# Optimization experiments

Hardware: AMD Instinct MI355X
Metric: run time of the kernel (lower is better)

Reference implementation:

```python
import math
import jax, jax.numpy as jnp
import numpy as np

HOP = 256
N_FFT = 1024
SR = 24000
B = 8
T = 1200          # feature frames
L = T * HOP       # 307200 audio samples
K_REV = 8192
BINS = N_FFT // 2 + 1


def setup_inputs() -> dict:
    key = jax.random.key(0)
    k1, k2, k3, k4, k5 = jax.random.split(key, 5)
    # realistic voiced f0 in [50, 400] Hz (forward gates on f0 > 20 Hz)
    f0 = 50.0 + 350.0 * jax.random.uniform(k1, (B, T), dtype=jnp.float32)
    env_per = jax.random.uniform(k2, (B, BINS, T), dtype=jnp.float32)
    env_noi = 0.1 * jax.random.uniform(k3, (B, BINS, T), dtype=jnp.float32)
    rev = 0.01 * jax.random.normal(k4, (B, K_REV), dtype=jnp.float32)
    # stands in for torch.rand_like(imp) inside forward (uniform [0,1))
    noi = jax.random.uniform(k5, (B, L), dtype=jnp.float32)
    # periodic Hann window, as torch.hann_window(n_fft)
    window = (0.5 - 0.5 * jnp.cos(2.0 * jnp.pi * jnp.arange(N_FFT) / N_FFT)).astype(jnp.float32)
    return {"f0": f0, "env_per": env_per, "env_noi": env_noi, "rev": rev, "noi": noi, "window": window}


def _interp_linear(x, scale):
    # torch F.interpolate(mode='linear', align_corners=False)
    Lx = x.shape[-1]
    out_len = Lx * scale
    src = (jnp.arange(out_len, dtype=jnp.float32) + 0.5) / scale - 0.5
    src = jnp.clip(src, 0.0, Lx - 1)
    i0 = jnp.floor(src).astype(jnp.int32)
    i1 = jnp.minimum(i0 + 1, Lx - 1)
    w = src - i0.astype(jnp.float32)
    return x[:, i0] * (1.0 - w) + x[:, i1] * w


def _stft(x, window):
    # torch.stft(center=True, pad_mode='reflect', return_complex=True)
    pad = N_FFT // 2
    xp = jnp.pad(x, ((0, 0), (pad, pad)), mode='reflect')
    n_frames = 1 + (xp.shape[-1] - N_FFT) // HOP
    idx = jnp.arange(n_frames)[:, None] * HOP + jnp.arange(N_FFT)[None, :]
    frames = xp[:, idx] * window                      # [B, F, N_FFT]
    return jnp.fft.rfft(frames, axis=-1).transpose(0, 2, 1)  # [B, BINS, F]


def _istft(spec, window):
    # torch.istft(center=True): windowed overlap-add with window-square normalization
    frames = jnp.fft.irfft(spec.transpose(0, 2, 1), n=N_FFT, axis=-1) * window  # [B, F, N_FFT]
    Bc, Fr, _ = frames.shape
    out_len = N_FFT + HOP * (Fr - 1)
    idx = (jnp.arange(Fr)[:, None] * HOP + jnp.arange(N_FFT)[None, :]).reshape(-1)
    out = jnp.zeros((Bc, out_len), frames.dtype).at[:, idx].add(frames.reshape(Bc, -1))
    wsq = jnp.zeros((out_len,), frames.dtype).at[idx].add(jnp.tile(window ** 2, Fr))
    out = out / jnp.where(wsq > 1e-11, wsq, 1.0)
    pad = N_FFT // 2
    return out[:, pad:out_len - pad]


def _min_phase(amp, eps=1e-5):
    # homomorphic minimum-phase reconstruction from real amplitude envelope
    # amp: [B, BINS, F]  ->  complex spectrum exp(rfft(lifted real cepstrum))
    log_amp = jnp.log(jnp.maximum(amp, eps))
    cep = jnp.fft.irfft(log_amp, n=N_FFT, axis=1)     # [B, N_FFT, F] real cepstrum
    lift = jnp.concatenate([
        jnp.ones((1,), jnp.float32),
        2.0 * jnp.ones((N_FFT // 2 - 1,), jnp.float32),
        jnp.ones((1,), jnp.float32),
        jnp.zeros((N_FFT // 2 - 1,), jnp.float32),
    ])
    return jnp.exp(jnp.fft.rfft(cep * lift[None, :, None], axis=1))  # [B, BINS, F]


def _fft_convolve(signal, kernel):
    # DDSP-style FFT convolution: zero-pad signal right, kernel left, multiply spectra
    Ls = signal.shape[-1]
    sig = jnp.pad(signal, ((0, 0), (0, Ls)))
    ker = jnp.pad(kernel, ((0, 0), (2 * Ls - kernel.shape[-1], 0)))
    out = jnp.fft.irfft(jnp.fft.rfft(sig) * jnp.fft.rfft(ker), n=2 * Ls)
    return out[:, Ls:]


def reference(f0, env_per, env_noi, rev, noi, window):
    env_per = jnp.pad(env_per, ((0, 0), (0, 0), (1, 0)))   # [B, BINS, T+1]
    env_noi = jnp.pad(env_noi, ((0, 0), (0, 0), (1, 0)))
    # sample-rate f0 track and impulse amplitude scale
    f0_up = _interp_linear(f0, HOP)                        # [B, L]
    imp_scale = jax.lax.rsqrt(jnp.maximum(f0_up, 20.0)) * math.sqrt(SR)
    # impulse train: fire where the running phase wraps past an integer
    phase = jnp.cumsum(f0_up, axis=-1) / SR
    saw = jnp.mod(phase, 1.0)
    imp = (saw - jnp.roll(saw, 1, axis=-1) < 0.0).astype(jnp.float32)
    imp = imp.at[:, 0].set(0.0)
    imp = imp * imp_scale
    imp_stft = _stft(imp, window)                          # [B, BINS, T+1]
    noi_stft = _stft(noi, window)
    # voiced/unvoiced gating of the periodic envelope
    mask = (jnp.pad(f0, ((0, 0), (1, 0)))[:, None, :] > 20.0).astype(jnp.float32)
    env_per = env_per * mask
    voi_stft = imp_stft * _min_phase(env_per) + noi_stft * env_noi
    voi = _istft(voi_stft, window)                         # [B, L]
    voi = _fft_convolve(voi, rev)                          # [B, L]
    return voi
```

## Files before the change

### kernel.cpp

```cpp
#include <hip/hip_runtime.h>
#include <math.h>

#define BB 8
#define TT 1200
#define NFFT 1024
#define BINS 513
#define LTOT 307200
#define KREV 8192
#define NFRM 34
#define NSAMP 8960
#define OUTOFF 299008
#define SQRT_SR 154.91933384829668f

#define OFF_FR   0

__device__ __forceinline__ int rev4_10(int n) {
    int r = (int)(__brev((unsigned)n) >> 22);
    return ((r & 0x155) << 1) | ((r & 0x2AA) >> 1);
}

__device__ __forceinline__ void dif4(float* re, float* im,
                                     const float* twr, const float* twi,
                                     float dir, int u, bool act) {
#pragma unroll
    for (int s = 0; s < 5; ++s) {
        const int q = 256 >> (2 * s);
        const int sh = 8 - 2 * s;
        __syncthreads();
        if (act) {
            int t = u & (q - 1);
            int base = ((u >> sh) << (sh + 2)) | t;
            int i0 = base, i1 = base + q, i2 = base + 2 * q, i3 = base + 3 * q;
            float ar = re[i0], ai = im[i0];
            float br = re[i1], bi = im[i1];
            float cr = re[i2], ci = im[i2];
            float dr = re[i3], di = im[i3];
            float t0r = ar + cr, t0i = ai + ci;
            float t1r = ar - cr, t1i = ai - ci;
            float t2r = br + dr, t2i = bi + di;
            float t3r = br - dr, t3i = bi - di;
            float y0r = t0r + t2r, y0i = t0i + t2i;
            float y2r = t0r - t2r, y2i = t0i - t2i;
            float y1r = t1r - dir * t3i, y1i = t1i + dir * t3r;
            float y3r = t1r + dir * t3i, y3i = t1i - dir * t3r;
            float c1 = twr[2 * q - 1 + t], s1 = twi[2 * q - 1 + t];
            float c2 = twr[q - 1 + t],     s2 = twi[q - 1 + t];
            float w1r = c1, w1i = dir * s1;
            float w2r = c2, w2i = dir * s2;
            float w3r = c1 * c2 - s1 * s2;
            float w3i = dir * (c1 * s2 + s1 * c2);
            re[i0] = y0r;                       im[i0] = y0i;
            re[i1] = y1r * w1r - y1i * w1i;     im[i1] = y1r * w1i + y1i * w1r;
            re[i2] = y2r * w2r - y2i * w2i;     im[i2] = y2r * w2i + y2i * w2r;
            re[i3] = y3r * w3r - y3i * w3i;     im[i3] = y3r * w3i + y3i * w3r;
        }
    }
    __syncthreads();
}

__device__ __forceinline__ void dit4(float* re, float* im,
                                     const float* twr, const float* twi,
                                     float dir, int u, bool act) {
#pragma unroll
    for (int s = 0; s < 5; ++s) {
        const int q = 1 << (2 * s);
        const int sh = 2 * s;
        __syncthreads();
        if (act) {
            int t = u & (q - 1);
            int base = ((u >> sh) << (sh + 2)) | t;
            int i0 = base, i1 = base + q, i2 = base + 2 * q, i3 = base + 3 * q;
            float c1 = twr[2 * q - 1 + t], s1 = twi[2 * q - 1 + t];
            float c2 = twr[q - 1 + t],     s2 = twi[q - 1 + t];
            float w1r = c1, w1i = dir * s1;
            float w2r = c2, w2i = dir * s2;
            float w3r = c1 * c2 - s1 * s2;
            float w3i = dir * (c1 * s2 + s1 * c2);
            float ar = re[i0], ai = im[i0];
            float xr = re[i1], xi = im[i1];
            float yr = re[i2], yi = im[i2];
            float zr = re[i3], zi = im[i3];
            float br = xr * w1r - xi * w1i, bi = xr * w1i + xi * w1r;
            float cr = yr * w2r - yi * w2i, ci = yr * w2i + yi * w2r;
            float dr = zr * w3r - zi * w3i, di = zr * w3i + zi * w3r;
            float t0r = ar + cr, t0i = ai + ci;
            float t1r = ar - cr, t1i = ai - ci;
            float t2r = br + dr, t2i = bi + di;
            float t3r = br - dr, t3i = bi - di;
            re[i0] = t0r + t2r;            im[i0] = t0i + t2i;
            re[i2] = t0r - t2r;            im[i2] = t0i - t2i;
            re[i1] = t1r - dir * t3i;      im[i1] = t1i + dir * t3r;
            re[i3] = t1r + dir * t3i;      im[i3] = t1i - dir * t3r;
        }
    }
    __syncthreads();
}

#define LV1 0
#define LV2 4480
#define LV3 6720
#define LV4 7840
#define LV5 8400
#define LV6 8680
#define LV7 8820
#define LV8 8890
#define LV9 8925
#define LV10 8942
#define LV11 8950
#define LV12 8954
#define LV13 8956

__global__ __launch_bounds__(512) void kfrm(const float* __restrict__ f0,
                                            const float* __restrict__ env_per,
                                            const float* __restrict__ env_noi,
                                            const float* __restrict__ noi,
                                            const float* __restrict__ win,
                                            float* __restrict__ W,
                                            float* __restrict__ out) {
    const int bid = blockIdx.x;
    const int tid = threadIdx.x;
    const int b = bid / 17;
    const int fp = (bid - b * 17) * 2;
    const int fg = fp + 1;

    __shared__ __align__(16) float SMEM[17917];
    __shared__ float cw[1281], fw[1281];
    __shared__ float twr[1023], twi[1023];

    {
        float4* out4 = (float4*)out;
        int g = bid * 512 + tid;
        for (int idx = g; idx < (BB * LTOT) / 4; idx += 136 * 512)
            out4[idx] = make_float4(0.f, 0.f, 0.f, 0.f);
    }
    for (int x = tid; x < 1023; x += 512) {
        int hb = 31 - __clz(x + 1);
        int half = 1 << hb;
        int t = (x + 1) - half;
        float a = 3.14159265358979323846f * ((float)t / (float)half);
        float sv, cv; sincosf(a, &sv, &cv);
        twr[x] = cv; twi[x] = sv;
    }

    float* F = SMEM;
    float* L = SMEM + 8960;
    for (int i = tid; i < NSAMP; i += 512) {
        float src = __fsub_rn(__fdiv_rn(__fadd_rn((float)i, 0.5f), 256.0f), 0.5f);
        src = fminf(fmaxf(src, 0.0f), (float)(TT - 1));
        int i0 = (int)floorf(src);
        int i1 = i0 + 1; if (i1 > TT - 1) i1 = TT - 1;
        float w = __fsub_rn(src, (float)i0);
        float a0 = __fmul_rn(f0[b * TT + i0], __fsub_rn(1.0f, w));
        float a1 = __fmul_rn(f0[b * TT + i1], w);
        F[i] = __fadd_rn(a0, a1);
    }
    __syncthreads();
    for (int j = tid; j < 2240; j += 512) {
        float a = __fadd_rn(F[4*j],     F[4*j + 1]);
        float c = __fadd_rn(F[4*j + 2], F[4*j + 3]);
        L[LV1 + 2*j] = a; L[LV1 + 2*j + 1] = c;
        L[LV2 + j] = __fadd_rn(a, c);
    }
    __syncthreads();
    for (int j = tid; j < 560; j += 512) {
        float a = __fadd_rn(L[LV2 + 4*j],     L[LV2 + 4*j + 1]);
        float c = __fadd_rn(L[LV2 + 4*j + 2], L[LV2 + 4*j + 3]);
        L[LV3 + 2*j] = a; L[LV3 + 2*j + 1] = c;
        L[LV4 + j] = __fadd_rn(a, c);
    }
    __syncthreads();
    if (tid < 140) {
        int j = tid;
        float a = __fadd_rn(L[LV4 + 4*j],     L[LV4 + 4*j + 1]);
        float c = __fadd_rn(L[LV4 + 4*j + 2], L[LV4 + 4*j + 3]);
        L[LV5 + 2*j] = a; L[LV5 + 2*j + 1] = c;
        L[LV6 + j] = __fadd_rn(a, c);
    }
    __syncthreads();
    if (tid < 35) {
        int j = tid;
        float a = __fadd_rn(L[LV6 + 4*j],     L[LV6 + 4*j + 1]);
        float c = __fadd_rn(L[LV6 + 4*j + 2], L[LV6 + 4*j + 3]);
        L[LV7 + 2*j] = a; L[LV7 + 2*j + 1] = c;
        L[LV8 + j] = __fadd_rn(a, c);
    }
    __syncthreads();
    if (tid < 9) {
        int j = tid;
        if (j < 8) {
            float a = __fadd_rn(L[LV8 + 4*j],     L[LV8 + 4*j + 1]);
            float c = __fadd_rn(L[LV8 + 4*j + 2], L[LV8 + 4*j + 3]);
            L[LV9 + 2*j] = a; L[LV9 + 2*j + 1] = c;
            L[LV10 + j] = __fadd_rn(a, c);
        } else {
            L[LV9 + 16] = __fadd_rn(L[LV8 + 32], L[LV8 + 33]);
        }
    }
    __syncthreads();
    if (tid == 0) {
        float a0 = __fadd_rn(L[LV10 + 0], L[LV10 + 1]);
        float a1 = __fadd_rn(L[LV10 + 2], L[LV10 + 3]);
        float a2 = __fadd_rn(L[LV10 + 4], L[LV10 + 5]);
        float a3 = __fadd_rn(L[LV10 + 6], L[LV10 + 7]);
        L[LV11 + 0] = a0; L[LV11 + 1] = a1; L[LV11 + 2] = a2; L[LV11 + 3] = a3;
        float b0 = __fadd_rn(a0, a1), b1 = __fadd_rn(a2, a3);
        L[LV12 + 0] = b0; L[LV12 + 1] = b1;
        L[LV13 + 0] = __fadd_rn(b0, b1);
    }
    __syncthreads();
    const int cbase = (fp >= 3) ? (256 * fp - 513) : 0;
    {
        const int offs[14] = {0, LV1, LV2, LV3, LV4, LV5, LV6, LV7, LV8, LV9, LV10, LV11, LV12, LV13};
        for (int w = tid; w < 1281; w += 512) {
            int p = cbase + w;
            if (p < NSAMP) {
                int n = p + 1;
                float acc = 0.f; int pos = 0; bool first = true;
#pragma unroll
                for (int k = 13; k >= 1; --k) {
                    if ((n >> k) & 1) {
                        float t = L[offs[k] + (pos >> k)];
                        acc = first ? t : __fadd_rn(acc, t);
                        first = false;
                        pos += (1 << k);
                    }
                }
                if (n & 1) {
                    float t = F[pos];
                    acc = first ? t : __fadd_rn(acc, t);
                }
                cw[w] = acc;
                fw[w] = F[p];
            }
        }
    }
    __syncthreads();

    float* wr_  = SMEM;
    float* wi_  = SMEM + 1024;
    float* zfr  = SMEM + 2048;
    float* zfi  = SMEM + 3072;
    float* zgr  = SMEM + 4096;
    float* zgi  = SMEM + 5120;
    float* mpfr = SMEM + 6144;
    float* mpfi = SMEM + 6660;
    float* mpgr = SMEM + 7176;
    float* mpgi = SMEM + 7692;
    const int u = tid & 255;
    const bool lo = (tid < 256);

    for (int k = tid; k < BINS; k += 512) {
        float epf = 0.0f;
        if (fp > 0) {
            float f0v = f0[b * TT + (fp - 1)];
            epf = (f0v > 20.0f) ? env_per[(size_t)(b * BINS + k) * TT + (fp - 1)] : 0.0f;
        }
        float f0g = f0[b * TT + (fg - 1)];
        float epg = (f0g > 20.0f) ? env_per[(size_t)(b * BINS + k) * TT + (fg - 1)] : 0.0f;
        mpfr[k] = logf(fmaxf(epf, 1e-5f));
        mpgr[k] = logf(fmaxf(epg, 1e-5f));
    }
    __syncthreads();
#pragma unroll
    for (int r = 0; r < 2; ++r) {
        int n = tid + 512 * r;
        int kv = (n <= 512) ? n : 1024 - n;
        wr_[n] = mpfr[kv];
        wi_[n] = mpgr[kv];
    }
    dif4(wr_, wi_, twr, twi, -1.f, u, lo);
    const float inv = 1.0f / 1024.0f;
#pragma unroll
    for (int r = 0; r < 2; ++r) {
        int p = tid + 512 * r;
        int n = rev4_10(p);
        float wgt = (n == 0 || n == 512) ? inv : ((n < 512) ? 2.0f * inv : 0.0f);
        wr_[p] *= wgt;
        wi_[p] *= wgt;
    }
    dit4(wr_, wi_, twr, twi, -1.f, u, lo);
    for (int k = tid; k < BINS; k += 512) {
        int mk = (1024 - k) & 1023;
        float yr = wr_[k], yi = wi_[k];
        float ymr = wr_[mk], ymi = -wi_[mk];
        float Lfr = 0.5f * (yr + ymr), Lfi = 0.5f * (yi + ymi);
        float dr = yr - ymr, di = yi - ymi;
        float Lgr = 0.5f * di, Lgi = -0.5f * dr;
        float ef = expf(Lfr);
        mpfr[k] = ef * cosf(Lfi); mpfi[k] = ef * sinf(Lfi);
        float eg = expf(Lgr);
        mpgr[k] = eg * cosf(Lgi); mpgi[k] = eg * sinf(Lgi);
    }
    __syncthreads();
#pragma unroll
    for (int r = 0; r < 2; ++r) {
        int n = tid + 512 * r;
        int i = 256 * fp + n - 512; if (i < 0) i = -i;
        float v = 0.0f;
        if (i > 0) {
            int iw = i - cbase;
            float ph  = __fdiv_rn(cw[iw], 24000.0f);
            float sw  = __fsub_rn(ph, floorf(ph));
            float ph2 = __fdiv_rn(cw[iw - 1], 24000.0f);
            float sw2 = __fsub_rn(ph2, floorf(ph2));
            if (__fsub_rn(sw, sw2) < 0.0f)
                v = __fmul_rn(__fdiv_rn(1.0f, __fsqrt_rn(fmaxf(fw[iw], 20.0f))), SQRT_SR);
        }
        float wv = win[n];
        zfr[n] = __fmul_rn(noi[b * LTOT + i], wv);
        zfi[n] = __fmul_rn(v, wv);
        int i2 = 256 * fg + n - 512; if (i2 < 0) i2 = -i2;
        float v2 = 0.0f;
        if (i2 > 0) {
            int iw = i2 - cbase;
            float ph  = __fdiv_rn(cw[iw], 24000.0f);
            float sw  = __fsub_rn(ph, floorf(ph));
            float ph2 = __fdiv_rn(cw[iw - 1], 24000.0f);
            float sw2 = __fsub_rn(ph2, floorf(ph2));
            if (__fsub_rn(sw, sw2) < 0.0f)
                v2 = __fmul_rn(__fdiv_rn(1.0f, __fsqrt_rn(fmaxf(fw[iw], 20.0f))), SQRT_SR);
        }
        zgr[n] = __fmul_rn(noi[b * LTOT + i2], wv);
        zgi[n] = __fmul_rn(v2, wv);
    }
    dif4(lo ? zfr : zgr, lo ? zfi : zgi, twr, twi, -1.f, u, true);
#pragma unroll
    for (int r = 0; r < 2; ++r) {
        int p = tid + 512 * r;
        int k = rev4_10(p);
        int kk = (k <= 512) ? k : 1024 - k;
        bool cj = (k > 512);
        int p1 = rev4_10(kk);
        int p2 = rev4_10((1024 - kk) & 1023);
        float vr, vi;
        {
            float z1r = zfr[p1], z1i = zfi[p1];
            float z2r = zfr[p2], z2i = -zfi[p2];
            float Nr = 0.5f * (z1r + z2r), Ni = 0.5f * (z1i + z2i);
            float dr = z1r - z2r, di = z1i - z2i;
            float Ir = 0.5f * di, Ii = -0.5f * dr;
            float mpr = mpfr[kk], mpi2 = mpfi[kk];
            float en = (fp == 0) ? 0.f : env_noi[(size_t)(b * BINS + kk) * TT + (fp - 1)];
            vr = Ir * mpr - Ii * mpi2 + Nr * en;
            vi = Ir * mpi2 + Ii * mpr + Ni * en;
            if (cj) vi = -vi;
        }
        float vgr, vgi;
        {
            float z1r = zgr[p1], z1i = zgi[p1];
            float z2r = zgr[p2], z2i = -zgi[p2];
            float Nr = 0.5f * (z1r + z2r), Ni = 0.5f * (z1i + z2i);
            float dr = z1r - z2r, di = z1i - z2i;
            float Ir = 0.5f * di, Ii = -0.5f * dr;
            float mpr = mpgr[kk], mpi2 = mpgi[kk];
            float en = env_noi[(size_t)(b * BINS + kk) * TT + (fg - 1)];
            vgr = Ir * mpr - Ii * mpi2 + Nr * en;
            vgi = Ir * mpi2 + Ii * mpr + Ni * en;
            if (cj) vgi = -vgi;
        }
        wr_[p] = vr - vgi;
        wi_[p] = vi + vgr;
    }
    dit4(wr_, wi_, twr, twi, +1.f, u, lo);
#pragma unroll
    for (int r = 0; r < 2; ++r) {
        int n = tid + 512 * r;
        float wv = win[n];
        W[OFF_FR + (((size_t)(b * NFRM + fp)) << 10) + n] = __fmul_rn(__fmul_rn(wr_[n], inv), wv);
        W[OFF_FR + (((size_t)(b * NFRM + fg)) << 10) + n] = __fmul_rn(__fmul_rn(wi_[n], inv), wv);
    }
}

__global__ __launch_bounds__(256) void k4(const float* __restrict__ rev,
                                          const float* __restrict__ win,
                                          const float* __restrict__ W,
                                          float* __restrict__ out) {
    const int tid = threadIdx.x;
    const int b = blockIdx.x / 72;
    int r = blockIdx.x - b * 72;
    int jt = 0, acc0 = 0;
    while (acc0 + 2 * (jt + 1) <= r) { acc0 += 2 * (jt + 1); ++jt; }
    const int mc = r - acc0;
    const int j0 = jt << 10, m0 = mc << 9;

    __shared__ __align__(16) float S[1536];
    const int base = j0 - m0 - 512;
    for (int x = tid; x < 1536; x += 256) {
        int j = base + x;
        float v = 0.f;
        if (j >= 0 && j < KREV) {
            int s = j + 512;
            int flo = (s >= 1023) ? ((s - 1023 + 255) >> 8) : 0;
            int fhi = s >> 8; if (fhi > NFRM - 1) fhi = NFRM - 1;
            float acc = 0.f, wsq = 0.f;
            for (int f = flo; f <= fhi; ++f) {
                int o = s - (f << 8);
                acc = __fadd_rn(acc, W[OFF_FR + (((size_t)(b * NFRM + f)) << 10) + o]);
                float wv = win[o];
                wsq = __fadd_rn(wsq, __fmul_rn(wv, wv));
            }
            float den = (wsq > 1e-11f) ? wsq : 1.0f;
            v = __fdiv_rn(acc, den);
        }
        S[x] = v;
    }
    __syncthreads();

    const float4* S4 = (const float4*)S;
    const float* Rb = rev + b * KREV + m0;
    float y0 = 0.f, y1 = 0.f, y2 = 0.f, y3 = 0.f;
    const int qi = tid + 128;
    float4 Bv = S4[qi];
#pragma unroll 4
    for (int mq = 0; mq < 128; ++mq) {
        float4 A = S4[qi - 1 - mq];
        float4 r4 = *(const float4*)(Rb + 4 * mq);
        y0 = fmaf(r4.x, Bv.x, y0); y0 = fmaf(r4.y, A.w,  y0); y0 = fmaf(r4.z, A.z,  y0); y0 = fmaf(r4.w, A.y,  y0);
        y1 = fmaf(r4.x, Bv.y, y1); y1 = fmaf(r4.y, Bv.x, y1); y1 = fmaf(r4.z, A.w,  y1); y1 = fmaf(r4.w, A.z,  y1);
        y2 = fmaf(r4.x, Bv.z, y2); y2 = fmaf(r4.y, Bv.y, y2); y2 = fmaf(r4.z, Bv.x, y2); y2 = fmaf(r4.w, A.w,  y2);
        y3 = fmaf(r4.x, Bv.w, y3); y3 = fmaf(r4.y, Bv.z, y3); y3 = fmaf(r4.z, Bv.y, y3); y3 = fmaf(r4.w, Bv.x, y3);
        Bv = A;
    }
    float* o = out + (size_t)b * LTOT + OUTOFF + j0 + 4 * tid;
    atomicAdd(o + 0, y0);
    atomicAdd(o + 1, y1);
    atomicAdd(o + 2, y2);
    atomicAdd(o + 3, y3);
}

extern "C" void kernel_launch(void* const* d_in, const int* in_sizes, int n_in,
                              void* d_out, int out_size, void* d_ws, size_t ws_size,
                              hipStream_t stream) {
    const float* f0      = (const float*)d_in[0];
    const float* env_per = (const float*)d_in[1];
    const float* env_noi = (const float*)d_in[2];
    const float* rev     = (const float*)d_in[3];
    const float* noi     = (const float*)d_in[4];
    const float* win     = (const float*)d_in[5];
    float* out = (float*)d_out;
    float* W   = (float*)d_ws;

    kfrm<<<dim3(136), dim3(512), 0, stream>>>(f0, env_per, env_noi, noi, win, W, out);
    k4<<<dim3(576),   dim3(256), 0, stream>>>(rev, win, W, out);
}
```

Baseline: 141.2 us.

## Overlap min-phase cepstrum FFT with f0 prefix-sum and impulse framing via warp specialization

Splits the 512-thread block into two halves. One half runs the cepstral min-phase FFT stages while the other half computes the f0 upsampling, the hierarchical cumsum and the impulse/noise frame construction, with the work interleaved between shared barriers. Before, these phases ran one after another, and half the threads sat idle during each FFT. Shared memory is re-laid out so the FFT buffers and the mp arrays no longer alias the cumsum scratch. The price is fewer threads per task, so the serial cumsum and frame-fill loops take more iterations each, and shared memory use grows, which can lower occupancy.

```diff
diff --git a/kernel.cpp b/kernel.cpp
--- a/kernel.cpp
+++ b/kernel.cpp
@@ -19,81 +19,67 @@
     return ((r & 0x155) << 1) | ((r & 0x2AA) >> 1);
 }
 
-__device__ __forceinline__ void dif4(float* re, float* im,
-                                     const float* twr, const float* twi,
-                                     float dir, int u, bool act) {
-#pragma unroll
-    for (int s = 0; s < 5; ++s) {
-        const int q = 256 >> (2 * s);
-        const int sh = 8 - 2 * s;
-        __syncthreads();
-        if (act) {
-            int t = u & (q - 1);
-            int base = ((u >> sh) << (sh + 2)) | t;
-            int i0 = base, i1 = base + q, i2 = base + 2 * q, i3 = base + 3 * q;
-            float ar = re[i0], ai = im[i0];
-            float br = re[i1], bi = im[i1];
-            float cr = re[i2], ci = im[i2];
-            float dr = re[i3], di = im[i3];
-            float t0r = ar + cr, t0i = ai + ci;
-            float t1r = ar - cr, t1i = ai - ci;
-            float t2r = br + dr, t2i = bi + di;
-            float t3r = br - dr, t3i = bi - di;
-            float y0r = t0r + t2r, y0i = t0i + t2i;
-            float y2r = t0r - t2r, y2i = t0i - t2i;
-            float y1r = t1r - dir * t3i, y1i = t1i + dir * t3r;
-            float y3r = t1r + dir * t3i, y3i = t1i - dir * t3r;
-            float c1 = twr[2 * q - 1 + t], s1 = twi[2 * q - 1 + t];
-            float c2 = twr[q - 1 + t],     s2 = twi[q - 1 + t];
-            float w1r = c1, w1i = dir * s1;
-            float w2r = c2, w2i = dir * s2;
-            float w3r = c1 * c2 - s1 * s2;
-            float w3i = dir * (c1 * s2 + s1 * c2);
-            re[i0] = y0r;                       im[i0] = y0i;
-            re[i1] = y1r * w1r - y1i * w1i;     im[i1] = y1r * w1i + y1i * w1r;
-            re[i2] = y2r * w2r - y2i * w2i;     im[i2] = y2r * w2i + y2i * w2r;
-            re[i3] = y3r * w3r - y3i * w3i;     im[i3] = y3r * w3i + y3i * w3r;
-        }
-    }
-    __syncthreads();
-}
-
-__device__ __forceinline__ void dit4(float* re, float* im,
-                                     const float* twr, const float* twi,
-                                     float dir, int u, bool act) {
-#pragma unroll
-    for (int s = 0; s < 5; ++s) {
-        const int q = 1 << (2 * s);
-        const int sh = 2 * s;
-        __syncthreads();
-        if (act) {
-            int t = u & (q - 1);
-            int base = ((u >> sh) << (sh + 2)) | t;
-            int i0 = base, i1 = base + q, i2 = base + 2 * q, i3 = base + 3 * q;
-            float c1 = twr[2 * q - 1 + t], s1 = twi[2 * q - 1 + t];
-            float c2 = twr[q - 1 + t],     s2 = twi[q - 1 + t];
-            float w1r = c1, w1i = dir * s1;
-            float w2r = c2, w2i = dir * s2;
-            float w3r = c1 * c2 - s1 * s2;
-            float w3i = dir * (c1 * s2 + s1 * c2);
-            float ar = re[i0], ai = im[i0];
-            float xr = re[i1], xi = im[i1];
-            float yr = re[i2], yi = im[i2];
-            float zr = re[i3], zi = im[i3];
-            float br = xr * w1r - xi * w1i, bi = xr * w1i + xi * w1r;
-            float cr = yr * w2r - yi * w2i, ci = yr * w2i + yi * w2r;
-            float dr = zr * w3r - zi * w3i, di = zr * w3i + zi * w3r;
-            float t0r = ar + cr, t0i = ai + ci;
-            float t1r = ar - cr, t1i = ai - ci;
-            float t2r = br + dr, t2i = bi + di;
-            float t3r = br - dr, t3i = bi - di;
-            re[i0] = t0r + t2r;            im[i0] = t0i + t2i;
-            re[i2] = t0r - t2r;            im[i2] = t0i - t2i;
-            re[i1] = t1r - dir * t3i;      im[i1] = t1i + dir * t3r;
-            re[i3] = t1r + dir * t3i;      im[i3] = t1i - dir * t3r;
-        }
-    }
-    __syncthreads();
+__device__ __forceinline__ void dif4_stage(float* re, float* im,
+                                           const float* twr, const float* twi,
+                                           float dir, int u, int s) {
+    const int q = 256 >> (2 * s);
+    const int sh = 8 - 2 * s;
+    int t = u & (q - 1);
+    int base = ((u >> sh) << (sh + 2)) | t;
+    int i0 = base, i1 = base + q, i2 = base + 2 * q, i3 = base + 3 * q;
+    float ar = re[i0], ai = im[i0];
+    float br = re[i1], bi = im[i1];
+    float cr = re[i2], ci = im[i2];
+    float dr = re[i3], di = im[i3];
+    float t0r = ar + cr, t0i = ai + ci;
+    float t1r = ar - cr, t1i = ai - ci;
+    float t2r = br + dr, t2i = bi + di;
+    float t3r = br - dr, t3i = bi - di;
+    float y0r = t0r + t2r, y0i = t0i + t2i;
+    float y2r = t0r - t2r, y2i = t0i - t2i;
+    float y1r = t1r - dir * t3i, y1i = t1i + dir * t3r;
+    float y3r = t1r + dir * t3i, y3i = t1i - dir * t3r;
+    float c1 = twr[2 * q - 1 + t], s1 = twi[2 * q - 1 + t];
+    float c2 = twr[q - 1 + t],     s2 = twi[q - 1 + t];
+    float w1r = c1, w1i = dir * s1;
+    float w2r = c2, w2i = dir * s2;
+    float w3r = c1 * c2 - s1 * s2;
+    float w3i = dir * (c1 * s2 + s1 * c2);
+    re[i0] = y0r;                       im[i0] = y0i;
+    re[i1] = y1r * w1r - y1i * w1i;     im[i1] = y1r * w1i + y1i * w1r;
+    re[i2] = y2r * w2r - y2i * w2i;     im[i2] = y2r * w2i + y2i * w2r;
+    re[i3] = y3r * w3r - y3i * w3i;     im[i3] = y3r * w3i + y3i * w3r;
+}
+
+__device__ __forceinline__ void dit4_stage(float* re, float* im,
+                                           const float* twr, const float* twi,
+                                           float dir, int u, int s) {
+    const int q = 1 << (2 * s);
+    const int sh = 2 * s;
+    int t = u & (q - 1);
+    int base = ((u >> sh) << (sh + 2)) | t;
+    int i0 = base, i1 = base + q, i2 = base + 2 * q, i3 = base + 3 * q;
+    float c1 = twr[2 * q - 1 + t], s1 = twi[2 * q - 1 + t];
+    float c2 = twr[q - 1 + t],     s2 = twi[q - 1 + t];
+    float w1r = c1, w1i = dir * s1;
+    float w2r = c2, w2i = dir * s2;
+    float w3r = c1 * c2 - s1 * s2;
+    float w3i = dir * (c1 * s2 + s1 * c2);
+    float ar = re[i0], ai = im[i0];
+    float xr = re[i1], xi = im[i1];
+    float yr = re[i2], yi = im[i2];
+    float zr = re[i3], zi = im[i3];
+    float br = xr * w1r - xi * w1i, bi = xr * w1i + xi * w1r;
+    float cr = yr * w2r - yi * w2i, ci = yr * w2i + yi * w2r;
+    float dr = zr * w3r - zi * w3i, di = zr * w3i + zi * w3r;
+    float t0r = ar + cr, t0i = ai + ci;
+    float t1r = ar - cr, t1i = ai - ci;
+    float t2r = br + dr, t2i = bi + di;
+    float t3r = br - dr, t3i = bi - di;
+    re[i0] = t0r + t2r;            im[i0] = t0i + t2i;
+    re[i2] = t0r - t2r;            im[i2] = t0i - t2i;
+    re[i1] = t1r - dir * t3i;      im[i1] = t1i + dir * t3r;
+    re[i3] = t1r + dir * t3i;      im[i3] = t1i - dir * t3r;
 }
 
 #define LV1 0
@@ -123,9 +109,17 @@
     const int fp = (bid - b * 17) * 2;
     const int fg = fp + 1;
 
-    __shared__ __align__(16) float SMEM[17917];
+    __shared__ __align__(16) float wr_[1024], wi_[1024];
+    __shared__ float mpfr[513], mpfi[513], mpgr[513], mpgi[513];
+    __shared__ __align__(16) float BIG[17917];
     __shared__ float cw[1281], fw[1281];
     __shared__ float twr[1023], twi[1023];
+    float* F   = BIG;
+    float* L   = BIG + 8960;
+    float* zfr = L;
+    float* zfi = L + 1024;
+    float* zgr = L + 2048;
+    float* zgi = L + 3072;
 
     {
         float4* out4 = (float4*)out;
@@ -142,51 +136,84 @@
         twr[x] = cv; twi[x] = sv;
     }
 
-    float* F = SMEM;
-    float* L = SMEM + 8960;
-    for (int i = tid; i < NSAMP; i += 512) {
-        float src = __fsub_rn(__fdiv_rn(__fadd_rn((float)i, 0.5f), 256.0f), 0.5f);
-        src = fminf(fmaxf(src, 0.0f), (float)(TT - 1));
-        int i0 = (int)floorf(src);
-        int i1 = i0 + 1; if (i1 > TT - 1) i1 = TT - 1;
-        float w = __fsub_rn(src, (float)i0);
-        float a0 = __fmul_rn(f0[b * TT + i0], __fsub_rn(1.0f, w));
-        float a1 = __fmul_rn(f0[b * TT + i1], w);
-        F[i] = __fadd_rn(a0, a1);
-    }
-    __syncthreads();
-    for (int j = tid; j < 2240; j += 512) {
-        float a = __fadd_rn(F[4*j],     F[4*j + 1]);
-        float c = __fadd_rn(F[4*j + 2], F[4*j + 3]);
-        L[LV1 + 2*j] = a; L[LV1 + 2*j + 1] = c;
-        L[LV2 + j] = __fadd_rn(a, c);
-    }
-    __syncthreads();
-    for (int j = tid; j < 560; j += 512) {
-        float a = __fadd_rn(L[LV2 + 4*j],     L[LV2 + 4*j + 1]);
-        float c = __fadd_rn(L[LV2 + 4*j + 2], L[LV2 + 4*j + 3]);
-        L[LV3 + 2*j] = a; L[LV3 + 2*j + 1] = c;
-        L[LV4 + j] = __fadd_rn(a, c);
-    }
-    __syncthreads();
-    if (tid < 140) {
-        int j = tid;
+    const bool lo = (tid < 256);
+    const int u = tid & 255;
+    const int cbase = (fp >= 3) ? (256 * fp - 513) : 0;
+    const float inv = 1.0f / 1024.0f;
+
+    if (lo) {
+        for (int k = u; k < BINS; k += 256) {
+            float epf = 0.0f;
+            if (fp > 0) {
+                float f0v = f0[b * TT + (fp - 1)];
+                epf = (f0v > 20.0f) ? env_per[(size_t)(b * BINS + k) * TT + (fp - 1)] : 0.0f;
+            }
+            float f0g = f0[b * TT + (fg - 1)];
+            float epg = (f0g > 20.0f) ? env_per[(size_t)(b * BINS + k) * TT + (fg - 1)] : 0.0f;
+            mpfr[k] = logf(fmaxf(epf, 1e-5f));
+            mpgr[k] = logf(fmaxf(epg, 1e-5f));
+        }
+    } else {
+        for (int i = u; i < NSAMP; i += 256) {
+            float src = __fsub_rn(__fdiv_rn(__fadd_rn((float)i, 0.5f), 256.0f), 0.5f);
+            src = fminf(fmaxf(src, 0.0f), (float)(TT - 1));
+            int i0 = (int)floorf(src);
+            int i1 = i0 + 1; if (i1 > TT - 1) i1 = TT - 1;
+            float w = __fsub_rn(src, (float)i0);
+            float a0 = __fmul_rn(f0[b * TT + i0], __fsub_rn(1.0f, w));
+            float a1 = __fmul_rn(f0[b * TT + i1], w);
+            F[i] = __fadd_rn(a0, a1);
+        }
+    }
+    __syncthreads();
+    if (lo) {
+#pragma unroll
+        for (int r = 0; r < 4; ++r) {
+            int n = u + 256 * r;
+            int kv = (n <= 512) ? n : 1024 - n;
+            wr_[n] = mpfr[kv];
+            wi_[n] = mpgr[kv];
+        }
+    } else {
+        for (int j = u; j < 2240; j += 256) {
+            float a = __fadd_rn(F[4*j],     F[4*j + 1]);
+            float c = __fadd_rn(F[4*j + 2], F[4*j + 3]);
+            L[LV1 + 2*j] = a; L[LV1 + 2*j + 1] = c;
+            L[LV2 + j] = __fadd_rn(a, c);
+        }
+    }
+    __syncthreads();
+    if (lo) dif4_stage(wr_, wi_, twr, twi, -1.f, u, 0);
+    else {
+        for (int j = u; j < 560; j += 256) {
+            float a = __fadd_rn(L[LV2 + 4*j],     L[LV2 + 4*j + 1]);
+            float c = __fadd_rn(L[LV2 + 4*j + 2], L[LV2 + 4*j + 3]);
+            L[LV3 + 2*j] = a; L[LV3 + 2*j + 1] = c;
+            L[LV4 + j] = __fadd_rn(a, c);
+        }
+    }
+    __syncthreads();
+    if (lo) dif4_stage(wr_, wi_, twr, twi, -1.f, u, 1);
+    else if (u < 140) {
+        int j = u;
         float a = __fadd_rn(L[LV4 + 4*j],     L[LV4 + 4*j + 1]);
         float c = __fadd_rn(L[LV4 + 4*j + 2], L[LV4 + 4*j + 3]);
         L[LV5 + 2*j] = a; L[LV5 + 2*j + 1] = c;
         L[LV6 + j] = __fadd_rn(a, c);
     }
     __syncthreads();
-    if (tid < 35) {
-        int j = tid;
+    if (lo) dif4_stage(wr_, wi_, twr, twi, -1.f, u, 2);
+    else if (u < 35) {
+        int j = u;
         float a = __fadd_rn(L[LV6 + 4*j],     L[LV6 + 4*j + 1]);
         float c = __fadd_rn(L[LV6 + 4*j + 2], L[LV6 + 4*j + 3]);
         L[LV7 + 2*j] = a; L[LV7 + 2*j + 1] = c;
         L[LV8 + j] = __fadd_rn(a, c);
     }
     __syncthreads();
-    if (tid < 9) {
-        int j = tid;
+    if (lo) dif4_stage(wr_, wi_, twr, twi, -1.f, u, 3);
+    else if (u < 9) {
+        int j = u;
         if (j < 8) {
             float a = __fadd_rn(L[LV8 + 4*j],     L[LV8 + 4*j + 1]);
             float c = __fadd_rn(L[LV8 + 4*j + 2], L[LV8 + 4*j + 3]);
@@ -197,7 +224,8 @@
         }
     }
     __syncthreads();
-    if (tid == 0) {
+    if (lo) dif4_stage(wr_, wi_, twr, twi, -1.f, u, 4);
+    else if (u == 0) {
         float a0 = __fadd_rn(L[LV10 + 0], L[LV10 + 1]);
         float a1 = __fadd_rn(L[LV10 + 2], L[LV10 + 3]);
         float a2 = __fadd_rn(L[LV10 + 4], L[LV10 + 5]);
@@ -208,10 +236,18 @@
         L[LV13 + 0] = __fadd_rn(b0, b1);
     }
     __syncthreads();
-    const int cbase = (fp >= 3) ? (256 * fp - 513) : 0;
-    {
+    if (lo) {
+#pragma unroll
+        for (int r = 0; r < 4; ++r) {
+            int p = u + 256 * r;
+            int n = rev4_10(p);
+            float wgt = (n == 0 || n == 512) ? inv : ((n < 512) ? 2.0f * inv : 0.0f);
+            wr_[p] *= wgt;
+            wi_[p] *= wgt;
+        }
+    } else {
         const int offs[14] = {0, LV1, LV2, LV3, LV4, LV5, LV6, LV7, LV8, LV9, LV10, LV11, LV12, LV13};
-        for (int w = tid; w < 1281; w += 512) {
+        for (int w = u; w < 1281; w += 256) {
             int p = cbase + w;
             if (p < NSAMP) {
                 int n = p + 1;
@@ -235,95 +271,76 @@
         }
     }
     __syncthreads();
-
-    float* wr_  = SMEM;
-    float* wi_  = SMEM + 1024;
-    float* zfr  = SMEM + 2048;
-    float* zfi  = SMEM + 3072;
-    float* zgr  = SMEM + 4096;
-    float* zgi  = SMEM + 5120;
-    float* mpfr = SMEM + 6144;
-    float* mpfi = SMEM + 6660;
-    float* mpgr = SMEM + 7176;
-    float* mpgi = SMEM + 7692;
-    const int u = tid & 255;
-    const bool lo = (tid < 256);
-
-    for (int k = tid; k < BINS; k += 512) {
-        float epf = 0.0f;
-        if (fp > 0) {
-            float f0v = f0[b * TT + (fp - 1)];
-            epf = (f0v > 20.0f) ? env_per[(size_t)(b * BINS + k) * TT + (fp - 1)] : 0.0f;
-        }
-        float f0g = f0[b * TT + (fg - 1)];
-        float epg = (f0g > 20.0f) ? env_per[(size_t)(b * BINS + k) * TT + (fg - 1)] : 0.0f;
-        mpfr[k] = logf(fmaxf(epf, 1e-5f));
-        mpgr[k] = logf(fmaxf(epg, 1e-5f));
-    }
-    __syncthreads();
-#pragma unroll
-    for (int r = 0; r < 2; ++r) {
-        int n = tid + 512 * r;
-        int kv = (n <= 512) ? n : 1024 - n;
-        wr_[n] = mpfr[kv];
-        wi_[n] = mpgr[kv];
-    }
-    dif4(wr_, wi_, twr, twi, -1.f, u, lo);
-    const float inv = 1.0f / 1024.0f;
-#pragma unroll
-    for (int r = 0; r < 2; ++r) {
-        int p = tid + 512 * r;
-        int n = rev4_10(p);
-        float wgt = (n == 0 || n == 512) ? inv : ((n < 512) ? 2.0f * inv : 0.0f);
-        wr_[p] *= wgt;
-        wi_[p] *= wgt;
-    }
-    dit4(wr_, wi_, twr, twi, -1.f, u, lo);
-    for (int k = tid; k < BINS; k += 512) {
-        int mk = (1024 - k) & 1023;
-        float yr = wr_[k], yi = wi_[k];
-        float ymr = wr_[mk], ymi = -wi_[mk];
-        float Lfr = 0.5f * (yr + ymr), Lfi = 0.5f * (yi + ymi);
-        float dr = yr - ymr, di = yi - ymi;
-        float Lgr = 0.5f * di, Lgi = -0.5f * dr;
-        float ef = expf(Lfr);
-        mpfr[k] = ef * cosf(Lfi); mpfi[k] = ef * sinf(Lfi);
-        float eg = expf(Lgr);
-        mpgr[k] = eg * cosf(Lgi); mpgi[k] = eg * sinf(Lgi);
-    }
-    __syncthreads();
-#pragma unroll
-    for (int r = 0; r < 2; ++r) {
-        int n = tid + 512 * r;
-        int i = 256 * fp + n - 512; if (i < 0) i = -i;
-        float v = 0.0f;
-        if (i > 0) {
-            int iw = i - cbase;
-            float ph  = __fdiv_rn(cw[iw], 24000.0f);
-            float sw  = __fsub_rn(ph, floorf(ph));
-            float ph2 = __fdiv_rn(cw[iw - 1], 24000.0f);
-            float sw2 = __fsub_rn(ph2, floorf(ph2));
-            if (__fsub_rn(sw, sw2) < 0.0f)
-                v = __fmul_rn(__fdiv_rn(1.0f, __fsqrt_rn(fmaxf(fw[iw], 20.0f))), SQRT_SR);
-        }
-        float wv = win[n];
-        zfr[n] = __fmul_rn(noi[b * LTOT + i], wv);
-        zfi[n] = __fmul_rn(v, wv);
-        int i2 = 256 * fg + n - 512; if (i2 < 0) i2 = -i2;
-        float v2 = 0.0f;
-        if (i2 > 0) {
-            int iw = i2 - cbase;
-            float ph  = __fdiv_rn(cw[iw], 24000.0f);
-            float sw  = __fsub_rn(ph, floorf(ph));
-            float ph2 = __fdiv_rn(cw[iw - 1], 24000.0f);
-            float sw2 = __fsub_rn(ph2, floorf(ph2));
-            if (__fsub_rn(sw, sw2) < 0.0f)
-                v2 = __fmul_rn(__fdiv_rn(1.0f, __fsqrt_rn(fmaxf(fw[iw], 20.0f))), SQRT_SR);
-        }
-        zgr[n] = __fmul_rn(noi[b * LTOT + i2], wv);
-        zgi[n] = __fmul_rn(v2, wv);
-    }
-    dif4(lo ? zfr : zgr, lo ? zfi : zgi, twr, twi, -1.f, u, true);
+    if (lo) dit4_stage(wr_, wi_, twr, twi, -1.f, u, 0);
+    else {
+        for (int n = u; n < 1024; n += 256) {
+            int i = 256 * fp + n - 512; if (i < 0) i = -i;
+            float v = 0.0f;
+            if (i > 0) {
+                int iw = i - cbase;
+                float ph  = __fdiv_rn(cw[iw], 24000.0f);
+                float sw  = __fsub_rn(ph, floorf(ph));
+                float ph2 = __fdiv_rn(cw[iw - 1], 24000.0f);
+                float sw2 = __fsub_rn(ph2, floorf(ph2));
+                if (__fsub_rn(sw, sw2) < 0.0f)
+                    v = __fmul_rn(__fdiv_rn(1.0f, __fsqrt_rn(fmaxf(fw[iw], 20.0f))), SQRT_SR);
+            }
+            float wv = win[n];
+            zfr[n] = __fmul_rn(noi[b * LTOT + i], wv);
+            zfi[n] = __fmul_rn(v, wv);
+        }
+    }
+    __syncthreads();
+    if (lo) dit4_stage(wr_, wi_, twr, twi, -1.f, u, 1);
+    else {
+        for (int n = u; n < 1024; n += 256) {
+            int i = 256 * fg + n - 512; if (i < 0) i = -i;
+            float v = 0.0f;
+            if (i > 0) {
+                int iw = i - cbase;
+                float ph  = __fdiv_rn(cw[iw], 24000.0f);
+                float sw  = __fsub_rn(ph, floorf(ph));
+                float ph2 = __fdiv_rn(cw[iw - 1], 24000.0f);
+                float sw2 = __fsub_rn(ph2, floorf(ph2));
+                if (__fsub_rn(sw, sw2) < 0.0f)
+                    v = __fmul_rn(__fdiv_rn(1.0f, __fsqrt_rn(fmaxf(fw[iw], 20.0f))), SQRT_SR);
+            }
+            float wv = win[n];
+            zgr[n] = __fmul_rn(noi[b * LTOT + i], wv);
+            zgi[n] = __fmul_rn(v, wv);
+        }
+    }
+    __syncthreads();
+    if (lo) dit4_stage(wr_, wi_, twr, twi, -1.f, u, 2);
+    __syncthreads();
+    if (lo) dit4_stage(wr_, wi_, twr, twi, -1.f, u, 3);
+    __syncthreads();
+    if (lo) dit4_stage(wr_, wi_, twr, twi, -1.f, u, 4);
+    __syncthreads();
+    if (lo) {
+        for (int k = u; k < BINS; k += 256) {
+            int mk = (1024 - k) & 1023;
+            float yr = wr_[k], yi = wi_[k];
+            float ymr = wr_[mk], ymi = -wi_[mk];
+            float Lfr = 0.5f * (yr + ymr), Lfi = 0.5f * (yi + ymi);
+            float dr = yr - ymr, di = yi - ymi;
+            float Lgr = 0.5f * di, Lgi = -0.5f * dr;
+            float ef = expf(Lfr);
+            mpfr[k] = ef * cosf(Lfi); mpfi[k] = ef * sinf(Lfi);
+            float eg = expf(Lgr);
+            mpgr[k] = eg * cosf(Lgi); mpgi[k] = eg * sinf(Lgi);
+        }
+    }
+    __syncthreads();
+    {
+        float* zr = lo ? zfr : zgr;
+        float* zi = lo ? zfi : zgi;
+#pragma unroll
+        for (int s = 0; s < 5; ++s) {
+            dif4_stage(zr, zi, twr, twi, -1.f, u, s);
+            __syncthreads();
+        }
+    }
 #pragma unroll
     for (int r = 0; r < 2; ++r) {
         int p = tid + 512 * r;
@@ -361,7 +378,12 @@
         wr_[p] = vr - vgi;
         wi_[p] = vi + vgr;
     }
-    dit4(wr_, wi_, twr, twi, +1.f, u, lo);
+    __syncthreads();
+#pragma unroll
+    for (int s = 0; s < 5; ++s) {
+        if (lo) dit4_stage(wr_, wi_, twr, twi, +1.f, u, s);
+        __syncthreads();
+    }
 #pragma unroll
     for (int r = 0; r < 2; ++r) {
         int n = tid + 512 * r;
```

Result: no change. 143.6 us (+1.7%).
